# Kernel optimization log

Measured on AMD Instinct MI355X. Metric: run time of the kernel, lower is better.

The kernel has to match this reference:

```python
import jax, jax.numpy as jnp
import numpy as np

N = 100000
D = 64
H = 4 * D  # 256
E = 1000000


def setup_inputs() -> dict:
    key = jax.random.key(0)
    ks = jax.random.split(key, 9)
    return {
        "loc_feat": jax.random.normal(ks[0], (N, D), dtype=jnp.float32),
        "geo_src": jax.random.randint(ks[1], (E,), 0, N),
        "geo_dst": jax.random.randint(ks[2], (E,), 0, N),
        "trans_src": jax.random.randint(ks[3], (E,), 0, N),
        "trans_dst": jax.random.randint(ks[4], (E,), 0, N),
        "trans_w": jax.random.uniform(ks[5], (E,), dtype=jnp.float32),
        "W1": jax.random.normal(ks[6], (D, H), dtype=jnp.float32) * (1.0 / np.sqrt(D)),
        "b1": jax.random.normal(ks[7], (H,), dtype=jnp.float32) * 0.01,
        "W2": jax.random.normal(ks[8], (H, 1), dtype=jnp.float32) * (1.0 / np.sqrt(H)),
    }


def reference(loc_feat, geo_src, geo_dst, trans_src, trans_dst, trans_w, W1, b1, W2):
    n = loc_feat.shape[0]
    # etype 'geo': copy_u + mean  -> segment mean of src features at dst
    geo_sum = jax.ops.segment_sum(loc_feat[geo_src], geo_dst, num_segments=n)
    cnt = jax.ops.segment_sum(jnp.ones(geo_src.shape[0], loc_feat.dtype), geo_dst, num_segments=n)
    geo = jnp.where(cnt[:, None] > 0, geo_sum / jnp.maximum(cnt, 1.0)[:, None], 0.0)
    # etype 'trans': u_mul_e + sum -> weighted segment sum
    trans = jax.ops.segment_sum(loc_feat[trans_src] * trans_w[:, None], trans_dst, num_segments=n)
    # semantic attention fuse over the two relation views
    z = jnp.stack([geo, trans], axis=1)          # [N, 2, D]
    h = jnp.tanh(jnp.einsum('nkd,dh->nkh', z, W1) + b1)  # [N, 2, H]
    w = jnp.einsum('nkh,ho->nko', h, W2).mean(0)  # [2, 1] (mean over nodes)
    beta = jax.nn.softmax(w, axis=0)              # [2, 1]
    return (beta[None, :, :] * z).sum(1)          # [N, D]
```

## Files before the change

### kernel.cpp

```cpp
#include <hip/hip_runtime.h>
#include <hip/hip_bf16.h>

#define N_NODES 100000
#define DIM 64
#define HID 256
#define E_EDGES 1000000
#define TWO_N (2 * N_NODES)

#define TILE 120
#define NBINS 834
#define CAP 1600
#define EPB 4096
#define FILL_BLOCKS 245
#define K1_FILL (2 * FILL_BLOCKS)
#define PACK_BLOCKS 3125
#define K1_GRID (K1_FILL + 1 + PACK_BLOCKS)

typedef short short8 __attribute__((ext_vector_type(8)));
typedef float f32x4 __attribute__((ext_vector_type(4)));
typedef unsigned short us4 __attribute__((ext_vector_type(4)));

#define ZSTRIDE 72

__device__ __forceinline__ float tanh_fast(float x) {
    x = fminf(fmaxf(x, -15.0f), 15.0f);
    float e = __expf(2.0f * x);
    return (e - 1.0f) / (e + 1.0f);
}

__device__ __forceinline__ unsigned short f2bf(float x) {
    unsigned u = __float_as_uint(x);
    u = u + 0x7FFFu + ((u >> 16) & 1u);
    return (unsigned short)(u >> 16);
}

__device__ __forceinline__ float bf2f(unsigned short u) {
    return __uint_as_float(((unsigned)u) << 16);
}

__global__ void __launch_bounds__(512) prep_kernel(
        const float* __restrict__ feat, unsigned short* __restrict__ fb,
        const float* __restrict__ W1, unsigned short* __restrict__ W1p,
        const int* __restrict__ gs, const int* __restrict__ gd,
        const int* __restrict__ ts, const int* __restrict__ td,
        const float* __restrict__ tw,
        int* __restrict__ gcount,
        int* __restrict__ gbin, int2* __restrict__ tbin) {
    __shared__ int   hist[NBINS];
    __shared__ int   adjS[NBINS];
    __shared__ int   curS[NBINS];
    __shared__ int   pS[EPB];
    __shared__ float w2S[EPB];
    __shared__ unsigned short binS[EPB];
    __shared__ int   wsumS[8];

    int t = threadIdx.x, lane = t & 63, wid = t >> 6;
    int b = blockIdx.x;

    if (b >= K1_FILL + 1) {
        int i = (b - K1_FILL - 1) * 512 + t;
        float4 v = ((const float4*)feat)[i];
        us4 o;
        o[0] = f2bf(v.x); o[1] = f2bf(v.y); o[2] = f2bf(v.z); o[3] = f2bf(v.w);
        ((us4*)fb)[i] = o;
        return;
    }
    if (b == K1_FILL) {
        for (int i = t; i < 16384; i += 512) {
            int j = i & 7;
            int r = i >> 3;
            int nidx = r & 15; r >>= 4;
            int q = r & 3; r >>= 2;
            int khalf = r & 1;
            int n = r >> 1;
            int k = 32 * khalf + 8 * q + j;
            int c = 16 * n + nidx;
            W1p[i] = f2bf(W1[k * HID + c]);
        }
        return;
    }

    int rel = (b >= FILL_BLOCKS) ? 1 : 0;
    int e0 = (rel ? b - FILL_BLOCKS : b) * EPB;
    const int* dstp = rel ? td : gd;
    const int* srcp = rel ? ts : gs;

    for (int i = t; i < NBINS; i += 512) hist[i] = 0;
    __syncthreads();

    int d_[8], s_[8];
    float w_[8];
    #pragma unroll
    for (int j = 0; j < 2; ++j) {
        int idx = e0 + j * 2048 + 4 * t;
        if (idx + 3 < E_EDGES) {
            int4 dv = *(const int4*)&dstp[idx];
            int4 sv = *(const int4*)&srcp[idx];
            d_[4*j+0] = dv.x; d_[4*j+1] = dv.y; d_[4*j+2] = dv.z; d_[4*j+3] = dv.w;
            s_[4*j+0] = sv.x; s_[4*j+1] = sv.y; s_[4*j+2] = sv.z; s_[4*j+3] = sv.w;
            if (rel) {
                float4 wv = *(const float4*)&tw[idx];
                w_[4*j+0] = wv.x; w_[4*j+1] = wv.y; w_[4*j+2] = wv.z; w_[4*j+3] = wv.w;
            }
        } else {
            #pragma unroll
            for (int i2 = 0; i2 < 4; ++i2) {
                bool ok = (idx + i2 < E_EDGES);
                d_[4*j+i2] = ok ? dstp[idx + i2] : -1;
                s_[4*j+i2] = ok ? srcp[idx + i2] : 0;
                w_[4*j+i2] = (ok && rel) ? tw[idx + i2] : 0.0f;
            }
        }
    }
    #pragma unroll
    for (int i = 0; i < 8; ++i)
        if (d_[i] >= 0) atomicAdd(&hist[d_[i] / TILE], 1);
    __syncthreads();

    int b0i = 2 * t, b1i = 2 * t + 1;
    int h0 = (b0i < NBINS) ? hist[b0i] : 0;
    int h1 = (b1i < NBINS) ? hist[b1i] : 0;
    int c = h0 + h1;
    int v = c;
    #pragma unroll
    for (int off = 1; off < 64; off <<= 1) {
        int u = __shfl_up(v, off);
        if (lane >= off) v += u;
    }
    if (lane == 63) wsumS[wid] = v;
    __syncthreads();
    if (t == 0) {
        int run = 0;
        #pragma unroll
        for (int i = 0; i < 8; ++i) { int x = wsumS[i]; wsumS[i] = run; run += x; }
    }
    __syncthreads();
    int excl = v - c + wsumS[wid];
    if (b0i < NBINS) {
        curS[b0i] = excl;
        int gb = (h0 > 0) ? (b0i * CAP + atomicAdd(&gcount[rel * NBINS + b0i], h0)) : 0;
        adjS[b0i] = gb - excl;
    }
    if (b1i < NBINS) {
        int lb1 = excl + h0;
        curS[b1i] = lb1;
        int gb = (h1 > 0) ? (b1i * CAP + atomicAdd(&gcount[rel * NBINS + b1i], h1)) : 0;
        adjS[b1i] = gb - lb1;
    }
    __syncthreads();

    #pragma unroll
    for (int i = 0; i < 8; ++i) {
        int d = d_[i];
        if (d < 0) continue;
        int bin = d / TILE;
        int pos = atomicAdd(&curS[bin], 1);
        pS[pos] = s_[i] | ((d - bin * TILE) << 20);
        binS[pos] = (unsigned short)bin;
        if (rel) w2S[pos] = w_[i];
    }
    __syncthreads();

    int nV = min(EPB, E_EDGES - e0);
    if (!rel) {
        for (int i = t; i < nV; i += 512) {
            int bb = binS[i];
            int gi = adjS[bb] + i;
            if (gi < (bb + 1) * CAP)
                gbin[gi] = pS[i];
        }
    } else {
        for (int i = t; i < nV; i += 512) {
            int bb = binS[i];
            int gi = adjS[bb] + i;
            if (gi < (bb + 1) * CAP)
                tbin[gi] = make_int2(pS[i], __float_as_int(w2S[i]));
        }
    }
}

__global__ void __launch_bounds__(256) agg_mlp_kernel(
        const unsigned short* __restrict__ featb,
        const int* __restrict__ gbin, const int2* __restrict__ tbin,
        const int* __restrict__ gcount,
        unsigned short* __restrict__ zb,
        const unsigned short* __restrict__ W1p,
        const float* __restrict__ bias1, const float* __restrict__ W2,
        float* __restrict__ sums, int* __restrict__ ticket,
        float* __restrict__ beta) {
    __shared__ int   srcS[CAP];
    __shared__ float wS[CAP];
    __shared__ int   histS[TILE];
    __shared__ int   baseS[TILE];
    __shared__ int   curS[TILE];
    __shared__ int   w0sum[1];
    __shared__ unsigned short zL[128 * ZSTRIDE];
    __shared__ float wred[4];

    int b = blockIdx.x;
    int rel = (b >= NBINS) ? 1 : 0;
    int bin = rel ? b - NBINS : b;
    int node0 = bin * TILE;
    int nNodes = min(TILE, N_NODES - node0);
    int t = threadIdx.x, lane = t & 63, wave = t >> 6;
    int q = lane >> 4, ql = lane & 15;

    int nE = gcount[b];
    if (nE > CAP) nE = CAP;

    for (int i = t; i < TILE; i += 256) histS[i] = 0;
    __syncthreads();

    if (!rel) {
        const int* bp = gbin + (size_t)bin * CAP;
        for (int i = t; i < nE; i += 256) atomicAdd(&histS[bp[i] >> 20], 1);
    } else {
        const int2* bp = tbin + (size_t)bin * CAP;
        for (int i = t; i < nE; i += 256) atomicAdd(&histS[bp[i].x >> 20], 1);
    }
    __syncthreads();

    int h = (t < TILE) ? histS[t] : 0;
    int v = h;
    #pragma unroll
    for (int off = 1; off < 64; off <<= 1) {
        int u = __shfl_up(v, off);
        if (lane >= off) v += u;
    }
    if (t == 63) w0sum[0] = v;
    __syncthreads();
    if (wave == 1) v += w0sum[0];
    if (t < TILE) {
        int base = v - h;
        baseS[t] = base;
        curS[t] = base;
    }
    __syncthreads();

    if (!rel) {
        const int* bp = gbin + (size_t)bin * CAP;
        for (int i = t; i < nE; i += 256) {
            int p = bp[i];
            int pos = atomicAdd(&curS[p >> 20], 1);
            srcS[pos] = p & 0xFFFFF;
        }
    } else {
        const int2* bp = tbin + (size_t)bin * CAP;
        for (int i = t; i < nE; i += 256) {
            int2 p = bp[i];
            int pos = atomicAdd(&curS[p.x >> 20], 1);
            srcS[pos] = p.x & 0xFFFFF;
            wS[pos] = __int_as_float(p.y);
        }
    }
    __syncthreads();

    for (int nl0 = wave * 4; nl0 < nNodes; nl0 += 16) {
        int nl = nl0 + q;
        bool act = (nl < nNodes);
        int deg = act ? histS[nl] : 0;
        int base = act ? baseS[nl] : 0;
        float a0 = 0.f, a1 = 0.f, a2 = 0.f, a3 = 0.f;
        if (!rel) {
            int k = 0;
            for (; k + 7 < deg; k += 8) {
                int s0 = srcS[base + k],     s1 = srcS[base + k + 1];
                int s2 = srcS[base + k + 2], s3 = srcS[base + k + 3];
                int s4 = srcS[base + k + 4], s5 = srcS[base + k + 5];
                int s6 = srcS[base + k + 6], s7 = srcS[base + k + 7];
                us4 r0 = *(const us4*)&featb[(size_t)s0 * DIM + ql * 4];
                us4 r1 = *(const us4*)&featb[(size_t)s1 * DIM + ql * 4];
                us4 r2 = *(const us4*)&featb[(size_t)s2 * DIM + ql * 4];
                us4 r3 = *(const us4*)&featb[(size_t)s3 * DIM + ql * 4];
                us4 r4 = *(const us4*)&featb[(size_t)s4 * DIM + ql * 4];
                us4 r5 = *(const us4*)&featb[(size_t)s5 * DIM + ql * 4];
                us4 r6 = *(const us4*)&featb[(size_t)s6 * DIM + ql * 4];
                us4 r7 = *(const us4*)&featb[(size_t)s7 * DIM + ql * 4];
                a0 += ((bf2f(r0[0]) + bf2f(r1[0])) + (bf2f(r2[0]) + bf2f(r3[0])))
                    + ((bf2f(r4[0]) + bf2f(r5[0])) + (bf2f(r6[0]) + bf2f(r7[0])));
                a1 += ((bf2f(r0[1]) + bf2f(r1[1])) + (bf2f(r2[1]) + bf2f(r3[1])))
                    + ((bf2f(r4[1]) + bf2f(r5[1])) + (bf2f(r6[1]) + bf2f(r7[1])));
                a2 += ((bf2f(r0[2]) + bf2f(r1[2])) + (bf2f(r2[2]) + bf2f(r3[2])))
                    + ((bf2f(r4[2]) + bf2f(r5[2])) + (bf2f(r6[2]) + bf2f(r7[2])));
                a3 += ((bf2f(r0[3]) + bf2f(r1[3])) + (bf2f(r2[3]) + bf2f(r3[3])))
                    + ((bf2f(r4[3]) + bf2f(r5[3])) + (bf2f(r6[3]) + bf2f(r7[3])));
            }
            for (; k + 1 < deg; k += 2) {
                int s0 = srcS[base + k], s1 = srcS[base + k + 1];
                us4 r0 = *(const us4*)&featb[(size_t)s0 * DIM + ql * 4];
                us4 r1 = *(const us4*)&featb[(size_t)s1 * DIM + ql * 4];
                a0 += bf2f(r0[0]) + bf2f(r1[0]);
                a1 += bf2f(r0[1]) + bf2f(r1[1]);
                a2 += bf2f(r0[2]) + bf2f(r1[2]);
                a3 += bf2f(r0[3]) + bf2f(r1[3]);
            }
            if (k < deg) {
                int s = srcS[base + k];
                us4 r = *(const us4*)&featb[(size_t)s * DIM + ql * 4];
                a0 += bf2f(r[0]); a1 += bf2f(r[1]);
                a2 += bf2f(r[2]); a3 += bf2f(r[3]);
            }
        } else {
            int k = 0;
            for (; k + 7 < deg; k += 8) {
                int s0 = srcS[base + k],     s1 = srcS[base + k + 1];
                int s2 = srcS[base + k + 2], s3 = srcS[base + k + 3];
                int s4 = srcS[base + k + 4], s5 = srcS[base + k + 5];
                int s6 = srcS[base + k + 6], s7 = srcS[base + k + 7];
                float w0 = wS[base + k],     w1 = wS[base + k + 1];
                float w2 = wS[base + k + 2], w3 = wS[base + k + 3];
                float w4 = wS[base + k + 4], w5 = wS[base + k + 5];
                float w6 = wS[base + k + 6], w7 = wS[base + k + 7];
                us4 r0 = *(const us4*)&featb[(size_t)s0 * DIM + ql * 4];
                us4 r1 = *(const us4*)&featb[(size_t)s1 * DIM + ql * 4];
                us4 r2 = *(const us4*)&featb[(size_t)s2 * DIM + ql * 4];
                us4 r3 = *(const us4*)&featb[(size_t)s3 * DIM + ql * 4];
                us4 r4 = *(const us4*)&featb[(size_t)s4 * DIM + ql * 4];
                us4 r5 = *(const us4*)&featb[(size_t)s5 * DIM + ql * 4];
                us4 r6 = *(const us4*)&featb[(size_t)s6 * DIM + ql * 4];
                us4 r7 = *(const us4*)&featb[(size_t)s7 * DIM + ql * 4];
                a0 += ((bf2f(r0[0])*w0 + bf2f(r1[0])*w1) + (bf2f(r2[0])*w2 + bf2f(r3[0])*w3))
                    + ((bf2f(r4[0])*w4 + bf2f(r5[0])*w5) + (bf2f(r6[0])*w6 + bf2f(r7[0])*w7));
                a1 += ((bf2f(r0[1])*w0 + bf2f(r1[1])*w1) + (bf2f(r2[1])*w2 + bf2f(r3[1])*w3))
                    + ((bf2f(r4[1])*w4 + bf2f(r5[1])*w5) + (bf2f(r6[1])*w6 + bf2f(r7[1])*w7));
                a2 += ((bf2f(r0[2])*w0 + bf2f(r1[2])*w1) + (bf2f(r2[2])*w2 + bf2f(r3[2])*w3))
                    + ((bf2f(r4[2])*w4 + bf2f(r5[2])*w5) + (bf2f(r6[2])*w6 + bf2f(r7[2])*w7));
                a3 += ((bf2f(r0[3])*w0 + bf2f(r1[3])*w1) + (bf2f(r2[3])*w2 + bf2f(r3[3])*w3))
                    + ((bf2f(r4[3])*w4 + bf2f(r5[3])*w5) + (bf2f(r6[3])*w6 + bf2f(r7[3])*w7));
            }
            for (; k + 1 < deg; k += 2) {
                int s0 = srcS[base + k], s1 = srcS[base + k + 1];
                float w0 = wS[base + k], w1 = wS[base + k + 1];
                us4 r0 = *(const us4*)&featb[(size_t)s0 * DIM + ql * 4];
                us4 r1 = *(const us4*)&featb[(size_t)s1 * DIM + ql * 4];
                a0 += bf2f(r0[0]) * w0 + bf2f(r1[0]) * w1;
                a1 += bf2f(r0[1]) * w0 + bf2f(r1[1]) * w1;
                a2 += bf2f(r0[2]) * w0 + bf2f(r1[2]) * w1;
                a3 += bf2f(r0[3]) * w0 + bf2f(r1[3]) * w1;
            }
            if (k < deg) {
                int s = srcS[base + k];
                float w = wS[base + k];
                us4 r = *(const us4*)&featb[(size_t)s * DIM + ql * 4];
                a0 += bf2f(r[0]) * w; a1 += bf2f(r[1]) * w;
                a2 += bf2f(r[2]) * w; a3 += bf2f(r[3]) * w;
            }
        }
        if (act) {
            float sc = rel ? 1.0f : 1.0f / fmaxf((float)deg, 1.0f);
            us4 o;
            o[0] = f2bf(a0 * sc); o[1] = f2bf(a1 * sc);
            o[2] = f2bf(a2 * sc); o[3] = f2bf(a3 * sc);
            size_t row = (size_t)(rel ? N_NODES + node0 + nl : node0 + nl);
            *(us4*)&zb[row * DIM + ql * 4] = o;
            *(us4*)&zL[nl * ZSTRIDE + ql * 4] = o;
        }
    }
    __syncthreads();

    int m = lane & 15;
    float csum = 0.0f;
    const short8* W1v = (const short8*)W1p;
    #pragma unroll
    for (int tt = 0; tt < 2; ++tt) {
        int rowbase = (wave * 2 + tt) * 16;
        short8 fa0 = *(const short8*)&zL[(rowbase + m) * ZSTRIDE + q * 8];
        short8 fa1 = *(const short8*)&zL[(rowbase + m) * ZSTRIDE + 32 + q * 8];
        #pragma unroll 4
        for (int n = 0; n < 16; ++n) {
            short8 fb0 = W1v[(n * 2 + 0) * 64 + lane];
            short8 fbK = W1v[(n * 2 + 1) * 64 + lane];
            f32x4 acc = {0.0f, 0.0f, 0.0f, 0.0f};
            acc = __builtin_amdgcn_mfma_f32_16x16x32_bf16(fa0, fb0, acc, 0, 0, 0);
            acc = __builtin_amdgcn_mfma_f32_16x16x32_bf16(fa1, fbK, acc, 0, 0, 0);
            int col = 16 * n + m;
            float bj = bias1[col];
            float w2 = W2[col];
            #pragma unroll
            for (int reg = 0; reg < 4; ++reg) {
                int nl = rowbase + q * 4 + reg;
                if (nl < nNodes) csum += tanh_fast(acc[reg] + bj) * w2;
            }
        }
    }
    #pragma unroll
    for (int off = 32; off > 0; off >>= 1) csum += __shfl_down(csum, off);
    if (lane == 0) wred[wave] = csum;
    __syncthreads();
    if (t == 0) {
        float cb = wred[0] + wred[1] + wred[2] + wred[3];
        atomicAdd(&sums[rel], cb);
        __threadfence();
        int old = atomicAdd(ticket, 1);
        if (old == 2 * NBINS - 1) {
            float s0 = atomicAdd(&sums[0], 0.0f) / (float)N_NODES;
            float s1 = atomicAdd(&sums[1], 0.0f) / (float)N_NODES;
            float mx = fmaxf(s0, s1);
            float e0 = __expf(s0 - mx), e1 = __expf(s1 - mx);
            float inv = 1.0f / (e0 + e1);
            beta[0] = e0 * inv;
            beta[1] = e1 * inv;
        }
    }
}

__global__ void combine_kernel(const unsigned short* __restrict__ zb,
                               const float* __restrict__ beta,
                               float* __restrict__ out) {
    int gid = blockIdx.x * 256 + threadIdx.x;
    float b0 = beta[0];
    float b1 = beta[1];
    uint4 g = *(const uint4*)&zb[(size_t)gid * 8];
    uint4 tr = *(const uint4*)&zb[(size_t)N_NODES * DIM + (size_t)gid * 8];
    float4 o0, o1;
    o0.x = b0 * __uint_as_float(g.x << 16) + b1 * __uint_as_float(tr.x << 16);
    o0.y = b0 * __uint_as_float(g.x & 0xFFFF0000u) + b1 * __uint_as_float(tr.x & 0xFFFF0000u);
    o0.z = b0 * __uint_as_float(g.y << 16) + b1 * __uint_as_float(tr.y << 16);
    o0.w = b0 * __uint_as_float(g.y & 0xFFFF0000u) + b1 * __uint_as_float(tr.y & 0xFFFF0000u);
    o1.x = b0 * __uint_as_float(g.z << 16) + b1 * __uint_as_float(tr.z << 16);
    o1.y = b0 * __uint_as_float(g.z & 0xFFFF0000u) + b1 * __uint_as_float(tr.z & 0xFFFF0000u);
    o1.z = b0 * __uint_as_float(g.w << 16) + b1 * __uint_as_float(tr.w << 16);
    o1.w = b0 * __uint_as_float(g.w & 0xFFFF0000u) + b1 * __uint_as_float(tr.w & 0xFFFF0000u);
    *(float4*)&out[(size_t)gid * 8] = o0;
    *(float4*)&out[(size_t)gid * 8 + 4] = o1;
}

extern "C" void kernel_launch(void* const* d_in, const int* in_sizes, int n_in,
                              void* d_out, int out_size, void* d_ws, size_t ws_size,
                              hipStream_t stream) {
    const float* loc_feat = (const float*)d_in[0];
    const int* geo_src    = (const int*)d_in[1];
    const int* geo_dst    = (const int*)d_in[2];
    const int* trans_src  = (const int*)d_in[3];
    const int* trans_dst  = (const int*)d_in[4];
    const float* trans_w  = (const float*)d_in[5];
    const float* W1       = (const float*)d_in[6];
    const float* b1       = (const float*)d_in[7];
    const float* W2       = (const float*)d_in[8];
    float* out = (float*)d_out;

    int*   gcount = (int*)d_ws;
    float* sums   = (float*)(gcount + 2 * NBINS);
    int*   ticket = (int*)(sums + 2);
    float* beta   = (float*)(ticket + 1);
    int*   gbin   = (int*)(beta + 2);
    int2*  tbin   = (int2*)(gbin + (size_t)NBINS * CAP);
    unsigned short* W1p   = (unsigned short*)(tbin + (size_t)NBINS * CAP);
    unsigned short* featb = W1p + 16384;
    unsigned short* zb    = featb + (size_t)N_NODES * DIM;

    hipMemsetAsync(d_ws, 0, (2 * NBINS + 5) * sizeof(int), stream);

    prep_kernel<<<K1_GRID, 512, 0, stream>>>(loc_feat, featb, W1, W1p,
                                             geo_src, geo_dst, trans_src, trans_dst,
                                             trans_w, gcount, gbin, tbin);
    agg_mlp_kernel<<<2 * NBINS, 256, 0, stream>>>(featb, gbin, tbin, gcount, zb,
                                                  W1p, b1, W2, sums, ticket, beta);
    combine_kernel<<<(N_NODES * DIM / 8) / 256, 256, 0, stream>>>(zb, beta, out);
}
```

Baseline: 264.8 us.

## Split fused aggregate+MLP kernel and shrink prep blocks to 256 threads

```diff
diff --git a/kernel.cpp b/kernel.cpp
--- a/kernel.cpp
+++ b/kernel.cpp
@@ -6,21 +6,20 @@
 #define HID 256
 #define E_EDGES 1000000
 #define TWO_N (2 * N_NODES)
+#define MLP_ROWBLOCKS (TWO_N / 64)
 
 #define TILE 120
 #define NBINS 834
 #define CAP 1600
-#define EPB 4096
-#define FILL_BLOCKS 245
-#define K1_FILL (2 * FILL_BLOCKS)
+#define EPB 2048
+#define FILL_PER_REL 489
+#define FILLB2 (2 * FILL_PER_REL)
 #define PACK_BLOCKS 3125
-#define K1_GRID (K1_FILL + 1 + PACK_BLOCKS)
+#define PREP_GRID (FILLB2 + 1 + PACK_BLOCKS)
 
 typedef short short8 __attribute__((ext_vector_type(8)));
 typedef float f32x4 __attribute__((ext_vector_type(4)));
 typedef unsigned short us4 __attribute__((ext_vector_type(4)));
-
-#define ZSTRIDE 72
 
 __device__ __forceinline__ float tanh_fast(float x) {
     x = fminf(fmaxf(x, -15.0f), 15.0f);
@@ -38,7 +37,7 @@
     return __uint_as_float(((unsigned)u) << 16);
 }
 
-__global__ void __launch_bounds__(512) prep_kernel(
+__global__ void __launch_bounds__(256) prep_kernel(
         const float* __restrict__ feat, unsigned short* __restrict__ fb,
         const float* __restrict__ W1, unsigned short* __restrict__ W1p,
         const int* __restrict__ gs, const int* __restrict__ gd,
@@ -52,21 +51,25 @@
     __shared__ int   pS[EPB];
     __shared__ float w2S[EPB];
     __shared__ unsigned short binS[EPB];
-    __shared__ int   wsumS[8];
+    __shared__ int   wsumS[4];
 
     int t = threadIdx.x, lane = t & 63, wid = t >> 6;
     int b = blockIdx.x;
 
-    if (b >= K1_FILL + 1) {
-        int i = (b - K1_FILL - 1) * 512 + t;
-        float4 v = ((const float4*)feat)[i];
-        us4 o;
-        o[0] = f2bf(v.x); o[1] = f2bf(v.y); o[2] = f2bf(v.z); o[3] = f2bf(v.w);
-        ((us4*)fb)[i] = o;
+    if (b >= FILLB2 + 1) {
+        int base = (b - FILLB2 - 1) * 512;
+        #pragma unroll
+        for (int r = 0; r < 2; ++r) {
+            int i = base + r * 256 + t;
+            float4 v = ((const float4*)feat)[i];
+            us4 o;
+            o[0] = f2bf(v.x); o[1] = f2bf(v.y); o[2] = f2bf(v.z); o[3] = f2bf(v.w);
+            ((us4*)fb)[i] = o;
+        }
         return;
     }
-    if (b == K1_FILL) {
-        for (int i = t; i < 16384; i += 512) {
+    if (b == FILLB2) {
+        for (int i = t; i < 16384; i += 256) {
             int j = i & 7;
             int r = i >> 3;
             int nidx = r & 15; r >>= 4;
@@ -80,19 +83,19 @@
         return;
     }
 
-    int rel = (b >= FILL_BLOCKS) ? 1 : 0;
-    int e0 = (rel ? b - FILL_BLOCKS : b) * EPB;
+    int rel = (b >= FILL_PER_REL) ? 1 : 0;
+    int e0 = (rel ? b - FILL_PER_REL : b) * EPB;
     const int* dstp = rel ? td : gd;
     const int* srcp = rel ? ts : gs;
 
-    for (int i = t; i < NBINS; i += 512) hist[i] = 0;
+    for (int i = t; i < NBINS; i += 256) hist[i] = 0;
     __syncthreads();
 
     int d_[8], s_[8];
     float w_[8];
     #pragma unroll
     for (int j = 0; j < 2; ++j) {
-        int idx = e0 + j * 2048 + 4 * t;
+        int idx = e0 + j * 1024 + 4 * t;
         if (idx + 3 < E_EDGES) {
             int4 dv = *(const int4*)&dstp[idx];
             int4 sv = *(const int4*)&srcp[idx];
@@ -117,10 +120,12 @@
         if (d_[i] >= 0) atomicAdd(&hist[d_[i] / TILE], 1);
     __syncthreads();
 
-    int b0i = 2 * t, b1i = 2 * t + 1;
-    int h0 = (b0i < NBINS) ? hist[b0i] : 0;
-    int h1 = (b1i < NBINS) ? hist[b1i] : 0;
-    int c = h0 + h1;
+    int myb = 4 * t;
+    int h0 = (myb + 0 < NBINS) ? hist[myb + 0] : 0;
+    int h1 = (myb + 1 < NBINS) ? hist[myb + 1] : 0;
+    int h2 = (myb + 2 < NBINS) ? hist[myb + 2] : 0;
+    int h3 = (myb + 3 < NBINS) ? hist[myb + 3] : 0;
+    int c = h0 + h1 + h2 + h3;
     int v = c;
     #pragma unroll
     for (int off = 1; off < 64; off <<= 1) {
@@ -132,20 +137,20 @@
     if (t == 0) {
         int run = 0;
         #pragma unroll
-        for (int i = 0; i < 8; ++i) { int x = wsumS[i]; wsumS[i] = run; run += x; }
-    }
-    __syncthreads();
-    int excl = v - c + wsumS[wid];
-    if (b0i < NBINS) {
-        curS[b0i] = excl;
-        int gb = (h0 > 0) ? (b0i * CAP + atomicAdd(&gcount[rel * NBINS + b0i], h0)) : 0;
-        adjS[b0i] = gb - excl;
-    }
-    if (b1i < NBINS) {
-        int lb1 = excl + h0;
-        curS[b1i] = lb1;
-        int gb = (h1 > 0) ? (b1i * CAP + atomicAdd(&gcount[rel * NBINS + b1i], h1)) : 0;
-        adjS[b1i] = gb - lb1;
+        for (int i = 0; i < 4; ++i) { int x = wsumS[i]; wsumS[i] = run; run += x; }
+    }
+    __syncthreads();
+    int run = v - c + wsumS[wid];
+    int hh[4] = {h0, h1, h2, h3};
+    #pragma unroll
+    for (int i = 0; i < 4; ++i) {
+        int bi = myb + i;
+        if (bi < NBINS) {
+            curS[bi] = run;
+            int gb = (hh[i] > 0) ? (bi * CAP + atomicAdd(&gcount[rel * NBINS + bi], hh[i])) : 0;
+            adjS[bi] = gb - run;
+            run += hh[i];
+        }
     }
     __syncthreads();
 
@@ -163,14 +168,14 @@
 
     int nV = min(EPB, E_EDGES - e0);
     if (!rel) {
-        for (int i = t; i < nV; i += 512) {
+        for (int i = t; i < nV; i += 256) {
             int bb = binS[i];
             int gi = adjS[bb] + i;
             if (gi < (bb + 1) * CAP)
                 gbin[gi] = pS[i];
         }
     } else {
-        for (int i = t; i < nV; i += 512) {
+        for (int i = t; i < nV; i += 256) {
             int bb = binS[i];
             int gi = adjS[bb] + i;
             if (gi < (bb + 1) * CAP)
@@ -179,23 +184,17 @@
     }
 }
 
-__global__ void __launch_bounds__(256) agg_mlp_kernel(
+__global__ void __launch_bounds__(256) aggregate_kernel(
         const unsigned short* __restrict__ featb,
         const int* __restrict__ gbin, const int2* __restrict__ tbin,
         const int* __restrict__ gcount,
-        unsigned short* __restrict__ zb,
-        const unsigned short* __restrict__ W1p,
-        const float* __restrict__ bias1, const float* __restrict__ W2,
-        float* __restrict__ sums, int* __restrict__ ticket,
-        float* __restrict__ beta) {
+        unsigned short* __restrict__ zb) {
     __shared__ int   srcS[CAP];
     __shared__ float wS[CAP];
     __shared__ int   histS[TILE];
     __shared__ int   baseS[TILE];
     __shared__ int   curS[TILE];
     __shared__ int   w0sum[1];
-    __shared__ unsigned short zL[128 * ZSTRIDE];
-    __shared__ float wred[4];
 
     int b = blockIdx.x;
     int rel = (b >= NBINS) ? 1 : 0;
@@ -353,46 +352,63 @@
             o[2] = f2bf(a2 * sc); o[3] = f2bf(a3 * sc);
             size_t row = (size_t)(rel ? N_NODES + node0 + nl : node0 + nl);
             *(us4*)&zb[row * DIM + ql * 4] = o;
-            *(us4*)&zL[nl * ZSTRIDE + ql * 4] = o;
-        }
-    }
-    __syncthreads();
-
-    int m = lane & 15;
-    float csum = 0.0f;
+        }
+    }
+}
+
+__global__ void __launch_bounds__(256) mlp_beta_kernel(
+        const unsigned short* __restrict__ zb,
+        const unsigned short* __restrict__ W1p,
+        const float* __restrict__ bias1, const float* __restrict__ W2,
+        float* __restrict__ sums, int* __restrict__ ticket,
+        float* __restrict__ beta) {
+    __shared__ float wred[4][2];
+    int t = threadIdx.x, lane = t & 63, wave = t >> 6;
+    int m = lane & 15, q = lane >> 4;
+    int base = blockIdx.x * 64 + wave * 16;
+    int R = base + m;
+
+    const unsigned short* rowp = zb + (size_t)R * DIM;
+    short8 a0 = *(const short8*)(rowp + q * 8);
+    short8 a1 = *(const short8*)(rowp + 32 + q * 8);
+
+    float c0 = 0.0f, c1 = 0.0f;
     const short8* W1v = (const short8*)W1p;
-    #pragma unroll
-    for (int tt = 0; tt < 2; ++tt) {
-        int rowbase = (wave * 2 + tt) * 16;
-        short8 fa0 = *(const short8*)&zL[(rowbase + m) * ZSTRIDE + q * 8];
-        short8 fa1 = *(const short8*)&zL[(rowbase + m) * ZSTRIDE + 32 + q * 8];
-        #pragma unroll 4
-        for (int n = 0; n < 16; ++n) {
-            short8 fb0 = W1v[(n * 2 + 0) * 64 + lane];
-            short8 fbK = W1v[(n * 2 + 1) * 64 + lane];
-            f32x4 acc = {0.0f, 0.0f, 0.0f, 0.0f};
-            acc = __builtin_amdgcn_mfma_f32_16x16x32_bf16(fa0, fb0, acc, 0, 0, 0);
-            acc = __builtin_amdgcn_mfma_f32_16x16x32_bf16(fa1, fbK, acc, 0, 0, 0);
-            int col = 16 * n + m;
-            float bj = bias1[col];
-            float w2 = W2[col];
-            #pragma unroll
-            for (int reg = 0; reg < 4; ++reg) {
-                int nl = rowbase + q * 4 + reg;
-                if (nl < nNodes) csum += tanh_fast(acc[reg] + bj) * w2;
-            }
-        }
-    }
-    #pragma unroll
-    for (int off = 32; off > 0; off >>= 1) csum += __shfl_down(csum, off);
-    if (lane == 0) wred[wave] = csum;
+
+    #pragma unroll 4
+    for (int n = 0; n < 16; ++n) {
+        short8 b0 = W1v[(n * 2 + 0) * 64 + lane];
+        short8 bK = W1v[(n * 2 + 1) * 64 + lane];
+        f32x4 acc = {0.0f, 0.0f, 0.0f, 0.0f};
+        acc = __builtin_amdgcn_mfma_f32_16x16x32_bf16(a0, b0, acc, 0, 0, 0);
+        acc = __builtin_amdgcn_mfma_f32_16x16x32_bf16(a1, bK, acc, 0, 0, 0);
+        int col = 16 * n + m;
+        float bj = bias1[col];
+        float w2 = W2[col];
+        #pragma unroll
+        for (int reg = 0; reg < 4; ++reg) {
+            int Rr = base + q * 4 + reg;
+            float h = tanh_fast(acc[reg] + bj);
+            float contrib = h * w2;
+            if (Rr < N_NODES) c0 += contrib; else c1 += contrib;
+        }
+    }
+
+    #pragma unroll
+    for (int off = 32; off > 0; off >>= 1) {
+        c0 += __shfl_down(c0, off);
+        c1 += __shfl_down(c1, off);
+    }
+    if (lane == 0) { wred[wave][0] = c0; wred[wave][1] = c1; }
     __syncthreads();
     if (t == 0) {
-        float cb = wred[0] + wred[1] + wred[2] + wred[3];
-        atomicAdd(&sums[rel], cb);
+        float p0 = wred[0][0] + wred[1][0] + wred[2][0] + wred[3][0];
+        float p1 = wred[0][1] + wred[1][1] + wred[2][1] + wred[3][1];
+        atomicAdd(&sums[0], p0);
+        atomicAdd(&sums[1], p1);
         __threadfence();
         int old = atomicAdd(ticket, 1);
-        if (old == 2 * NBINS - 1) {
+        if (old == MLP_ROWBLOCKS - 1) {
             float s0 = atomicAdd(&sums[0], 0.0f) / (float)N_NODES;
             float s1 = atomicAdd(&sums[1], 0.0f) / (float)N_NODES;
             float mx = fmaxf(s0, s1);
@@ -451,10 +467,10 @@
 
     hipMemsetAsync(d_ws, 0, (2 * NBINS + 5) * sizeof(int), stream);
 
-    prep_kernel<<<K1_GRID, 512, 0, stream>>>(loc_feat, featb, W1, W1p,
-                                             geo_src, geo_dst, trans_src, trans_dst,
-                                             trans_w, gcount, gbin, tbin);
-    agg_mlp_kernel<<<2 * NBINS, 256, 0, stream>>>(featb, gbin, tbin, gcount, zb,
-                                                  W1p, b1, W2, sums, ticket, beta);
+    prep_kernel<<<PREP_GRID, 256, 0, stream>>>(loc_feat, featb, W1, W1p,
+                                               geo_src, geo_dst, trans_src, trans_dst,
+                                               trans_w, gcount, gbin, tbin);
+    aggregate_kernel<<<2 * NBINS, 256, 0, stream>>>(featb, gbin, tbin, gcount, zb);
+    mlp_beta_kernel<<<MLP_ROWBLOCKS, 256, 0, stream>>>(zb, W1p, b1, W2, sums, ticket, beta);
     combine_kernel<<<(N_NODES * DIM / 8) / 256, 256, 0, stream>>>(zb, beta, out);
 }
```

Measured after the change: 360.4 us. +36.1%, slower.

## Bin edges into coarse 960-node buckets and filter per sub-tile in aggregation

Applied to the files above, without the earlier changes.

```diff
diff --git a/kernel.cpp b/kernel.cpp
--- a/kernel.cpp
+++ b/kernel.cpp
@@ -7,20 +7,22 @@
 #define E_EDGES 1000000
 #define TWO_N (2 * N_NODES)
 
+#define COARSE 960
+#define NCOARSE 105
+#define CCAP 10560
 #define TILE 120
-#define NBINS 834
+#define SUBS 8
 #define CAP 1600
 #define EPB 4096
-#define FILL_BLOCKS 245
-#define K1_FILL (2 * FILL_BLOCKS)
+#define FILL_PER_REL 245
+#define FILLB2 (2 * FILL_PER_REL)
 #define PACK_BLOCKS 3125
-#define K1_GRID (K1_FILL + 1 + PACK_BLOCKS)
+#define PREP_GRID (FILLB2 + 1 + PACK_BLOCKS)
+#define AGG_GRID (2 * NCOARSE * SUBS)
 
 typedef short short8 __attribute__((ext_vector_type(8)));
 typedef float f32x4 __attribute__((ext_vector_type(4)));
 typedef unsigned short us4 __attribute__((ext_vector_type(4)));
-
-#define ZSTRIDE 72
 
 __device__ __forceinline__ float tanh_fast(float x) {
     x = fminf(fmaxf(x, -15.0f), 15.0f);
@@ -46,26 +48,25 @@
         const float* __restrict__ tw,
         int* __restrict__ gcount,
         int* __restrict__ gbin, int2* __restrict__ tbin) {
-    __shared__ int   hist[NBINS];
-    __shared__ int   adjS[NBINS];
-    __shared__ int   curS[NBINS];
+    __shared__ int   hist[NCOARSE];
+    __shared__ int   adjS[NCOARSE];
+    __shared__ int   curS[NCOARSE];
     __shared__ int   pS[EPB];
     __shared__ float w2S[EPB];
-    __shared__ unsigned short binS[EPB];
-    __shared__ int   wsumS[8];
-
-    int t = threadIdx.x, lane = t & 63, wid = t >> 6;
+    __shared__ unsigned char binS[EPB];
+
+    int t = threadIdx.x, lane = t & 63;
     int b = blockIdx.x;
 
-    if (b >= K1_FILL + 1) {
-        int i = (b - K1_FILL - 1) * 512 + t;
+    if (b >= FILLB2 + 1) {
+        int i = (b - FILLB2 - 1) * 512 + t;
         float4 v = ((const float4*)feat)[i];
         us4 o;
         o[0] = f2bf(v.x); o[1] = f2bf(v.y); o[2] = f2bf(v.z); o[3] = f2bf(v.w);
         ((us4*)fb)[i] = o;
         return;
     }
-    if (b == K1_FILL) {
+    if (b == FILLB2) {
         for (int i = t; i < 16384; i += 512) {
             int j = i & 7;
             int r = i >> 3;
@@ -80,12 +81,12 @@
         return;
     }
 
-    int rel = (b >= FILL_BLOCKS) ? 1 : 0;
-    int e0 = (rel ? b - FILL_BLOCKS : b) * EPB;
+    int rel = (b >= FILL_PER_REL) ? 1 : 0;
+    int e0 = (rel ? b - FILL_PER_REL : b) * EPB;
     const int* dstp = rel ? td : gd;
     const int* srcp = rel ? ts : gs;
 
-    for (int i = t; i < NBINS; i += 512) hist[i] = 0;
+    for (int i = t; i < NCOARSE; i += 512) hist[i] = 0;
     __syncthreads();
 
     int d_[8], s_[8];
@@ -114,38 +115,32 @@
     }
     #pragma unroll
     for (int i = 0; i < 8; ++i)
-        if (d_[i] >= 0) atomicAdd(&hist[d_[i] / TILE], 1);
-    __syncthreads();
-
-    int b0i = 2 * t, b1i = 2 * t + 1;
-    int h0 = (b0i < NBINS) ? hist[b0i] : 0;
-    int h1 = (b1i < NBINS) ? hist[b1i] : 0;
-    int c = h0 + h1;
-    int v = c;
-    #pragma unroll
-    for (int off = 1; off < 64; off <<= 1) {
-        int u = __shfl_up(v, off);
-        if (lane >= off) v += u;
-    }
-    if (lane == 63) wsumS[wid] = v;
-    __syncthreads();
-    if (t == 0) {
-        int run = 0;
+        if (d_[i] >= 0) atomicAdd(&hist[d_[i] / COARSE], 1);
+    __syncthreads();
+
+    if (t < 64) {
+        int b0i = 2 * t, b1i = 2 * t + 1;
+        int h0 = (b0i < NCOARSE) ? hist[b0i] : 0;
+        int h1 = (b1i < NCOARSE) ? hist[b1i] : 0;
+        int c = h0 + h1;
+        int v = c;
         #pragma unroll
-        for (int i = 0; i < 8; ++i) { int x = wsumS[i]; wsumS[i] = run; run += x; }
-    }
-    __syncthreads();
-    int excl = v - c + wsumS[wid];
-    if (b0i < NBINS) {
-        curS[b0i] = excl;
-        int gb = (h0 > 0) ? (b0i * CAP + atomicAdd(&gcount[rel * NBINS + b0i], h0)) : 0;
-        adjS[b0i] = gb - excl;
-    }
-    if (b1i < NBINS) {
-        int lb1 = excl + h0;
-        curS[b1i] = lb1;
-        int gb = (h1 > 0) ? (b1i * CAP + atomicAdd(&gcount[rel * NBINS + b1i], h1)) : 0;
-        adjS[b1i] = gb - lb1;
+        for (int off = 1; off < 64; off <<= 1) {
+            int u = __shfl_up(v, off);
+            if (lane >= off) v += u;
+        }
+        int excl = v - c;
+        if (b0i < NCOARSE) {
+            curS[b0i] = excl;
+            int gb = (h0 > 0) ? (b0i * CCAP + atomicAdd(&gcount[rel * NCOARSE + b0i], h0)) : 0;
+            adjS[b0i] = gb - excl;
+        }
+        if (b1i < NCOARSE) {
+            int lb1 = excl + h0;
+            curS[b1i] = lb1;
+            int gb = (h1 > 0) ? (b1i * CCAP + atomicAdd(&gcount[rel * NCOARSE + b1i], h1)) : 0;
+            adjS[b1i] = gb - lb1;
+        }
     }
     __syncthreads();
 
@@ -153,10 +148,10 @@
     for (int i = 0; i < 8; ++i) {
         int d = d_[i];
         if (d < 0) continue;
-        int bin = d / TILE;
+        int bin = d / COARSE;
         int pos = atomicAdd(&curS[bin], 1);
-        pS[pos] = s_[i] | ((d - bin * TILE) << 20);
-        binS[pos] = (unsigned short)bin;
+        pS[pos] = s_[i] | ((d - bin * COARSE) << 20);
+        binS[pos] = (unsigned char)bin;
         if (rel) w2S[pos] = w_[i];
     }
     __syncthreads();
@@ -166,14 +161,14 @@
         for (int i = t; i < nV; i += 512) {
             int bb = binS[i];
             int gi = adjS[bb] + i;
-            if (gi < (bb + 1) * CAP)
+            if (gi < (bb + 1) * CCAP)
                 gbin[gi] = pS[i];
         }
     } else {
         for (int i = t; i < nV; i += 512) {
             int bb = binS[i];
             int gi = adjS[bb] + i;
-            if (gi < (bb + 1) * CAP)
+            if (gi < (bb + 1) * CCAP)
                 tbin[gi] = make_int2(pS[i], __float_as_int(w2S[i]));
         }
     }
@@ -186,37 +181,48 @@
         unsigned short* __restrict__ zb,
         const unsigned short* __restrict__ W1p,
         const float* __restrict__ bias1, const float* __restrict__ W2,
-        float* __restrict__ sums, int* __restrict__ ticket,
-        float* __restrict__ beta) {
+        float* __restrict__ partials) {
     __shared__ int   srcS[CAP];
     __shared__ float wS[CAP];
     __shared__ int   histS[TILE];
     __shared__ int   baseS[TILE];
     __shared__ int   curS[TILE];
     __shared__ int   w0sum[1];
-    __shared__ unsigned short zL[128 * ZSTRIDE];
     __shared__ float wred[4];
 
     int b = blockIdx.x;
-    int rel = (b >= NBINS) ? 1 : 0;
-    int bin = rel ? b - NBINS : b;
-    int node0 = bin * TILE;
+    int rel = (b >= NCOARSE * SUBS) ? 1 : 0;
+    int idx = rel ? b - NCOARSE * SUBS : b;
+    int coarse = idx >> 3, sub = idx & 7;
+    int node0 = coarse * COARSE + sub * TILE;
     int nNodes = min(TILE, N_NODES - node0);
     int t = threadIdx.x, lane = t & 63, wave = t >> 6;
     int q = lane >> 4, ql = lane & 15;
 
-    int nE = gcount[b];
-    if (nE > CAP) nE = CAP;
+    if (nNodes <= 0) {
+        if (t == 0) partials[b] = 0.0f;
+        return;
+    }
+
+    int nE = gcount[rel * NCOARSE + coarse];
+    if (nE > CCAP) nE = CCAP;
+    int lo = sub * TILE, hi = lo + nNodes;
 
     for (int i = t; i < TILE; i += 256) histS[i] = 0;
     __syncthreads();
 
     if (!rel) {
-        const int* bp = gbin + (size_t)bin * CAP;
-        for (int i = t; i < nE; i += 256) atomicAdd(&histS[bp[i] >> 20], 1);
+        const int* seg = gbin + (size_t)coarse * CCAP;
+        for (int i = t; i < nE; i += 256) {
+            int dl = seg[i] >> 20;
+            if (dl >= lo && dl < hi) atomicAdd(&histS[dl - lo], 1);
+        }
     } else {
-        const int2* bp = tbin + (size_t)bin * CAP;
-        for (int i = t; i < nE; i += 256) atomicAdd(&histS[bp[i].x >> 20], 1);
+        const int2* seg = tbin + (size_t)coarse * CCAP;
+        for (int i = t; i < nE; i += 256) {
+            int dl = seg[i].x >> 20;
+            if (dl >= lo && dl < hi) atomicAdd(&histS[dl - lo], 1);
+        }
     }
     __syncthreads();
 
@@ -238,19 +244,27 @@
     __syncthreads();
 
     if (!rel) {
-        const int* bp = gbin + (size_t)bin * CAP;
+        const int* seg = gbin + (size_t)coarse * CCAP;
         for (int i = t; i < nE; i += 256) {
-            int p = bp[i];
-            int pos = atomicAdd(&curS[p >> 20], 1);
-            srcS[pos] = p & 0xFFFFF;
+            int p = seg[i];
+            int dl = p >> 20;
+            if (dl >= lo && dl < hi) {
+                int pos = atomicAdd(&curS[dl - lo], 1);
+                if (pos < CAP) srcS[pos] = p & 0xFFFFF;
+            }
         }
     } else {
-        const int2* bp = tbin + (size_t)bin * CAP;
+        const int2* seg = tbin + (size_t)coarse * CCAP;
         for (int i = t; i < nE; i += 256) {
-            int2 p = bp[i];
-            int pos = atomicAdd(&curS[p.x >> 20], 1);
-            srcS[pos] = p.x & 0xFFFFF;
-            wS[pos] = __int_as_float(p.y);
+            int2 p = seg[i];
+            int dl = p.x >> 20;
+            if (dl >= lo && dl < hi) {
+                int pos = atomicAdd(&curS[dl - lo], 1);
+                if (pos < CAP) {
+                    srcS[pos] = p.x & 0xFFFFF;
+                    wS[pos] = __int_as_float(p.y);
+                }
+            }
         }
     }
     __syncthreads();
@@ -260,6 +274,8 @@
         bool act = (nl < nNodes);
         int deg = act ? histS[nl] : 0;
         int base = act ? baseS[nl] : 0;
+        if (base > CAP) base = CAP;
+        if (base + deg > CAP) deg = CAP - base;
         float a0 = 0.f, a1 = 0.f, a2 = 0.f, a3 = 0.f;
         if (!rel) {
             int k = 0;
@@ -285,16 +301,7 @@
                 a3 += ((bf2f(r0[3]) + bf2f(r1[3])) + (bf2f(r2[3]) + bf2f(r3[3])))
                     + ((bf2f(r4[3]) + bf2f(r5[3])) + (bf2f(r6[3]) + bf2f(r7[3])));
             }
-            for (; k + 1 < deg; k += 2) {
-                int s0 = srcS[base + k], s1 = srcS[base + k + 1];
-                us4 r0 = *(const us4*)&featb[(size_t)s0 * DIM + ql * 4];
-                us4 r1 = *(const us4*)&featb[(size_t)s1 * DIM + ql * 4];
-                a0 += bf2f(r0[0]) + bf2f(r1[0]);
-                a1 += bf2f(r0[1]) + bf2f(r1[1]);
-                a2 += bf2f(r0[2]) + bf2f(r1[2]);
-                a3 += bf2f(r0[3]) + bf2f(r1[3]);
-            }
-            if (k < deg) {
+            for (; k < deg; ++k) {
                 int s = srcS[base + k];
                 us4 r = *(const us4*)&featb[(size_t)s * DIM + ql * 4];
                 a0 += bf2f(r[0]); a1 += bf2f(r[1]);
@@ -328,17 +335,7 @@
                 a3 += ((bf2f(r0[3])*w0 + bf2f(r1[3])*w1) + (bf2f(r2[3])*w2 + bf2f(r3[3])*w3))
                     + ((bf2f(r4[3])*w4 + bf2f(r5[3])*w5) + (bf2f(r6[3])*w6 + bf2f(r7[3])*w7));
             }
-            for (; k + 1 < deg; k += 2) {
-                int s0 = srcS[base + k], s1 = srcS[base + k + 1];
-                float w0 = wS[base + k], w1 = wS[base + k + 1];
-                us4 r0 = *(const us4*)&featb[(size_t)s0 * DIM + ql * 4];
-                us4 r1 = *(const us4*)&featb[(size_t)s1 * DIM + ql * 4];
-                a0 += bf2f(r0[0]) * w0 + bf2f(r1[0]) * w1;
-                a1 += bf2f(r0[1]) * w0 + bf2f(r1[1]) * w1;
-                a2 += bf2f(r0[2]) * w0 + bf2f(r1[2]) * w1;
-                a3 += bf2f(r0[3]) * w0 + bf2f(r1[3]) * w1;
-            }
-            if (k < deg) {
+            for (; k < deg; ++k) {
                 int s = srcS[base + k];
                 float w = wS[base + k];
                 us4 r = *(const us4*)&featb[(size_t)s * DIM + ql * 4];
@@ -353,7 +350,6 @@
             o[2] = f2bf(a2 * sc); o[3] = f2bf(a3 * sc);
             size_t row = (size_t)(rel ? N_NODES + node0 + nl : node0 + nl);
             *(us4*)&zb[row * DIM + ql * 4] = o;
-            *(us4*)&zL[nl * ZSTRIDE + ql * 4] = o;
         }
     }
     __syncthreads();
@@ -363,9 +359,12 @@
     const short8* W1v = (const short8*)W1p;
     #pragma unroll
     for (int tt = 0; tt < 2; ++tt) {
-        int rowbase = (wave * 2 + tt) * 16;
-        short8 fa0 = *(const short8*)&zL[(rowbase + m) * ZSTRIDE + q * 8];
-        short8 fa1 = *(const short8*)&zL[(rowbase + m) * ZSTRIDE + 32 + q * 8];
+        int rowbase = wave * 32 + tt * 16;
+        long gr = (long)(rel ? N_NODES + node0 : node0) + rowbase + m;
+        if (gr > (long)TWO_N - 1) gr = (long)TWO_N - 1;
+        const unsigned short* rowp = zb + (size_t)gr * DIM;
+        short8 fa0 = *(const short8*)(rowp + q * 8);
+        short8 fa1 = *(const short8*)(rowp + 32 + q * 8);
         #pragma unroll 4
         for (int n = 0; n < 16; ++n) {
             short8 fb0 = W1v[(n * 2 + 0) * 64 + lane];
@@ -387,29 +386,36 @@
     for (int off = 32; off > 0; off >>= 1) csum += __shfl_down(csum, off);
     if (lane == 0) wred[wave] = csum;
     __syncthreads();
-    if (t == 0) {
-        float cb = wred[0] + wred[1] + wred[2] + wred[3];
-        atomicAdd(&sums[rel], cb);
-        __threadfence();
-        int old = atomicAdd(ticket, 1);
-        if (old == 2 * NBINS - 1) {
-            float s0 = atomicAdd(&sums[0], 0.0f) / (float)N_NODES;
-            float s1 = atomicAdd(&sums[1], 0.0f) / (float)N_NODES;
-            float mx = fmaxf(s0, s1);
-            float e0 = __expf(s0 - mx), e1 = __expf(s1 - mx);
-            float inv = 1.0f / (e0 + e1);
-            beta[0] = e0 * inv;
-            beta[1] = e1 * inv;
-        }
-    }
-}
-
-__global__ void combine_kernel(const unsigned short* __restrict__ zb,
-                               const float* __restrict__ beta,
-                               float* __restrict__ out) {
-    int gid = blockIdx.x * 256 + threadIdx.x;
-    float b0 = beta[0];
-    float b1 = beta[1];
+    if (t == 0) partials[b] = wred[0] + wred[1] + wred[2] + wred[3];
+}
+
+__global__ void __launch_bounds__(256) combine_kernel(
+        const unsigned short* __restrict__ zb,
+        const float* __restrict__ partials,
+        float* __restrict__ out) {
+    __shared__ float red[4][2];
+    int t = threadIdx.x, lane = t & 63, wv = t >> 6;
+
+    float c0 = 0.0f, c1 = 0.0f;
+    for (int i = t; i < AGG_GRID; i += 256) {
+        float p = partials[i];
+        if (i < NCOARSE * SUBS) c0 += p; else c1 += p;
+    }
+    #pragma unroll
+    for (int off = 32; off > 0; off >>= 1) {
+        c0 += __shfl_down(c0, off);
+        c1 += __shfl_down(c1, off);
+    }
+    if (lane == 0) { red[wv][0] = c0; red[wv][1] = c1; }
+    __syncthreads();
+    float s0 = (red[0][0] + red[1][0] + red[2][0] + red[3][0]) / (float)N_NODES;
+    float s1 = (red[0][1] + red[1][1] + red[2][1] + red[3][1]) / (float)N_NODES;
+    float mx = fmaxf(s0, s1);
+    float e0 = __expf(s0 - mx), e1 = __expf(s1 - mx);
+    float inv = 1.0f / (e0 + e1);
+    float b0 = e0 * inv, b1 = e1 * inv;
+
+    int gid = blockIdx.x * 256 + t;
     uint4 g = *(const uint4*)&zb[(size_t)gid * 8];
     uint4 tr = *(const uint4*)&zb[(size_t)N_NODES * DIM + (size_t)gid * 8];
     float4 o0, o1;
@@ -439,22 +445,20 @@
     const float* W2       = (const float*)d_in[8];
     float* out = (float*)d_out;
 
-    int*   gcount = (int*)d_ws;
-    float* sums   = (float*)(gcount + 2 * NBINS);
-    int*   ticket = (int*)(sums + 2);
-    float* beta   = (float*)(ticket + 1);
-    int*   gbin   = (int*)(beta + 2);
-    int2*  tbin   = (int2*)(gbin + (size_t)NBINS * CAP);
-    unsigned short* W1p   = (unsigned short*)(tbin + (size_t)NBINS * CAP);
+    int*   gcount   = (int*)d_ws;
+    float* partials = (float*)(gcount + 2 * NCOARSE);
+    int*   gbin     = (int*)(partials + AGG_GRID);
+    int2*  tbin     = (int2*)(gbin + (size_t)NCOARSE * CCAP);
+    unsigned short* W1p   = (unsigned short*)(tbin + (size_t)NCOARSE * CCAP);
     unsigned short* featb = W1p + 16384;
     unsigned short* zb    = featb + (size_t)N_NODES * DIM;
 
-    hipMemsetAsync(d_ws, 0, (2 * NBINS + 5) * sizeof(int), stream);
-
-    prep_kernel<<<K1_GRID, 512, 0, stream>>>(loc_feat, featb, W1, W1p,
-                                             geo_src, geo_dst, trans_src, trans_dst,
-                                             trans_w, gcount, gbin, tbin);
-    agg_mlp_kernel<<<2 * NBINS, 256, 0, stream>>>(featb, gbin, tbin, gcount, zb,
-                                                  W1p, b1, W2, sums, ticket, beta);
-    combine_kernel<<<(N_NODES * DIM / 8) / 256, 256, 0, stream>>>(zb, beta, out);
-}
+    hipMemsetAsync(gcount, 0, 2 * NCOARSE * sizeof(int), stream);
+
+    prep_kernel<<<PREP_GRID, 512, 0, stream>>>(loc_feat, featb, W1, W1p,
+                                               geo_src, geo_dst, trans_src, trans_dst,
+                                               trans_w, gcount, gbin, tbin);
+    agg_mlp_kernel<<<AGG_GRID, 256, 0, stream>>>(featb, gbin, tbin, gcount, zb,
+                                                 W1p, b1, W2, partials);
+    combine_kernel<<<(N_NODES * DIM / 8) / 256, 256, 0, stream>>>(zb, partials, out);
+}
```

New measurement: 255.4 us. 1.04x faster.
